# Kernel tuning notes

Hardware: AMD Instinct MI355X
Metric: run time of the kernel (lower is better)

Reference implementation:

```python
import jax, jax.numpy as jnp
import numpy as np

B, N, D = 8, 4096, 6          # clouds, points per cloud, coordinate dim
K = 64                        # max_num_neighbors in radius query
NS1, NS2 = 2048, 512          # fps ratios 0.5 and 0.25
R1, R2 = 0.2, 0.4             # ball-query radii
DIMS = {1: [6, 64, 64, 128], 2: [134, 128, 128, 256], 3: [262, 256, 512, 1024], 4: [1024, 512, 512]}


def setup_inputs():
    key = jax.random.key(0)
    k0, k1, k2 = jax.random.split(key, 3)
    inp = {}
    inp['synapse_cordi'] = jax.random.normal(k0, (B * N, D), jnp.float32)
    inp['batch_index'] = jnp.repeat(jnp.arange(B, dtype=jnp.int32), N)
    inp['weight'] = jax.random.uniform(k1, (B * N,), jnp.float32)
    k = k2
    for i, dims in DIMS.items():
        for j in range(len(dims) - 1):
            k, kw = jax.random.split(k)
            inp[f'w{i}_{j}'] = jax.random.normal(kw, (dims[j], dims[j + 1]), jnp.float32) * (1.0 / float(np.sqrt(dims[j])))
            inp[f'b{i}_{j}'] = jnp.zeros((dims[j + 1],), jnp.float32)
    return inp


def _mlp(x, params):
    # PyG MLP, plain_last=True; batch-norm at default (eval, running stats) is identity
    n = len(params)
    for i, (W, b) in enumerate(params):
        x = x @ W + b
        if i < n - 1:
            x = jax.nn.relu(x)
    return x


def _fps(pos, n_s):
    # farthest point sampling on one cloud [N, D] -> [n_s] indices (deterministic start at 0)
    d0 = jnp.sum((pos - pos[0]) ** 2, axis=-1)
    def step(mind, _):
        nxt = jnp.argmax(mind)
        mind = jnp.minimum(mind, jnp.sum((pos - pos[nxt]) ** 2, axis=-1))
        return mind, nxt
    _, idxs = jax.lax.scan(step, d0, None, length=n_s - 1)
    return jnp.concatenate([jnp.zeros((1,), idxs.dtype), idxs])


def _ball(pos, pos_q, r):
    # radius query: up to K nearest points within r for each query; [n_q,K] idx + validity mask
    d2 = jnp.sum((pos_q[:, None, :] - pos[None, :, :]) ** 2, axis=-1)  # [n_q, N]
    neg = jnp.where(d2 <= r * r, -d2, -jnp.inf)
    vals, nbr = jax.lax.top_k(neg, K)
    return nbr, vals > -jnp.inf


def _sa(x, pos, params, n_s, r):
    # Weight_Sample_Module: fps -> radius -> PointNetConv (gather, MLP, masked max-scatter)
    idx = jax.vmap(lambda p: _fps(p, n_s))(pos)                     # [B, n_s]
    pos_q = jnp.take_along_axis(pos, idx[..., None], axis=1)        # [B, n_s, D]
    nbr, valid = jax.vmap(lambda p, q: _ball(p, q, r))(pos, pos_q)  # [B, n_s, K]
    gather = lambda a: jax.vmap(lambda t, i: t[i])(a, nbr)          # [B, n_s, K, C]
    rel = gather(pos) - pos_q[:, :, None, :]
    feat = rel if x is None else jnp.concatenate([gather(x), rel], axis=-1)
    h = _mlp(feat, params)                                          # [B, n_s, K, C_out]
    h = jnp.where(valid[..., None], h, -jnp.inf)
    return jnp.max(h, axis=2), pos_q                                # max aggregation


def reference(synapse_cordi, batch_index, weight,
              w1_0, b1_0, w1_1, b1_1, w1_2, b1_2,
              w2_0, b2_0, w2_1, b2_1, w2_2, b2_2,
              w3_0, b3_0, w3_1, b3_1, w3_2, b3_2,
              w4_0, b4_0, w4_1, b4_1):
    pos = synapse_cordi.reshape(B, N, D)  # uniform clouds; batch_index = repeat(arange(B), N)
    p1 = [(w1_0, b1_0), (w1_1, b1_1), (w1_2, b1_2)]
    p2 = [(w2_0, b2_0), (w2_1, b2_1), (w2_2, b2_2)]
    p3 = [(w3_0, b3_0), (w3_1, b3_1), (w3_2, b3_2)]
    p4 = [(w4_0, b4_0), (w4_1, b4_1)]
    x1, pos1 = _sa(None, pos, p1, NS1, R1)   # [B, 2048, 128]
    x2, pos2 = _sa(x1, pos1, p2, NS2, R2)    # [B, 512, 256]
    h = _mlp(jnp.concatenate([x2, pos2], axis=-1), p3)  # [B, 512, 1024]
    g = jnp.max(h, axis=1)                   # global max pool -> [B, 1024]
    return _mlp(g, p4)                       # [B, 512]
```

## Files before the change

### kernel.cpp

```cpp
#include <hip/hip_runtime.h>
#include <math.h>

#define B_ 8
#define N_ 4096
#define D_ 6
#define K_ 64
#define NS1_ 2048
#define NS2_ 512

typedef float v2f __attribute__((ext_vector_type(2)));


__device__ __forceinline__ float dist2_rn(const float* __restrict__ a, const float* __restrict__ q) {
    float s = 0.f;
#pragma unroll
    for (int d = 0; d < 6; ++d) {
        float diff = __fsub_rn(a[d], q[d]);
        s = __fadd_rn(s, __fmul_rn(diff, diff));
    }
    return s;
}

__device__ __forceinline__ unsigned mapf(float x) {
    unsigned u = __float_as_uint(x);
    return (u & 0x80000000u) ? ~u : (u | 0x80000000u);
}
__device__ __forceinline__ float unmapf(unsigned u) {
    return __uint_as_float((u & 0x80000000u) ? (u & 0x7FFFFFFFu) : ~u);
}

template <int CTRL>
__device__ __forceinline__ double dppd(double k) {
    int lo = __double2loint(k), hi = __double2hiint(k);
    int nlo = __builtin_amdgcn_update_dpp(lo, lo, CTRL, 0xF, 0xF, false);
    int nhi = __builtin_amdgcn_update_dpp(hi, hi, CTRL, 0xF, 0xF, false);
    return __hiloint2double(nhi, nlo);
}


__device__ __forceinline__ void wait_flag(unsigned* f, int t) {
    if (t == 0) {
        while (__hip_atomic_load(f, __ATOMIC_RELAXED, __HIP_MEMORY_SCOPE_AGENT) == 0u)
            __builtin_amdgcn_s_sleep(32);
        __builtin_amdgcn_fence(__ATOMIC_ACQUIRE, "agent");
    }
    __syncthreads();
}


template <int NP, int NS>
__device__ __forceinline__ void fps_core(float* __restrict__ spos, int* __restrict__ sidx,
                                         double* __restrict__ part, int t) {
#pragma clang fp contract(off)
    constexpr int NT = 256;
    constexpr int P = NP / NT;
    constexpr int HP = P / 2;
    int lane = t & 63, w = t >> 6;

    v2f px2[HP][6];
#pragma unroll
    for (int j = 0; j < HP; ++j)
#pragma unroll
        for (int d = 0; d < 6; ++d) {
            px2[j][d].x = spos[(t + NT * (2 * j)) * 6 + d];
            px2[j][d].y = spos[(t + NT * (2 * j + 1)) * 6 + d];
        }

    float cx[6];
#pragma unroll
    for (int d = 0; d < 6; ++d) cx[d] = spos[d];

    v2f mind2[HP];
    float runv = -1.f;
    int runj = 0;
#pragma unroll
    for (int j = 0; j < HP; ++j) {
        v2f d2 = {0.f, 0.f};
#pragma unroll
        for (int d = 0; d < 6; ++d) {
            v2f df = px2[j][d] - cx[d];
            d2 = d2 + df * df;
        }
        mind2[j] = d2;
        if (d2.x > runv) { runv = d2.x; runj = t + NT * (2 * j); }
        if (d2.y > runv) { runv = d2.y; runj = t + NT * (2 * j + 1); }
    }

    for (int s = 1; s < NS; ++s) {
        double key = __hiloint2double((int)__float_as_uint(runv), (int)(unsigned)(~runj));
        key = fmax(key, dppd<0x111>(key));
        key = fmax(key, dppd<0x112>(key));
        key = fmax(key, dppd<0x114>(key));
        key = fmax(key, dppd<0x118>(key));
        key = fmax(key, dppd<0x142>(key));
        key = fmax(key, dppd<0x143>(key));
        if (lane == 63) part[(s & 1) * 4 + w] = key;
        __syncthreads();
        double kk = part[(s & 1) * 4 + (lane & 3)];
        kk = fmax(kk, dppd<0x111>(kk));
        kk = fmax(kk, dppd<0x112>(kk));
        int nx = ~__builtin_amdgcn_readlane(__double2loint(kk), 3);
        if (t == 0) sidx[s] = nx;

        const float2* sv2 = (const float2*)spos;
        float2 ca = sv2[nx * 3], cb = sv2[nx * 3 + 1], cc = sv2[nx * 3 + 2];
        cx[0] = ca.x; cx[1] = ca.y; cx[2] = cb.x; cx[3] = cb.y; cx[4] = cc.x; cx[5] = cc.y;

        runv = -1.f;
        runj = 0;
#pragma unroll
        for (int j = 0; j < HP; ++j) {
            v2f d2 = {0.f, 0.f};
#pragma unroll
            for (int d = 0; d < 6; ++d) {
                v2f df = px2[j][d] - cx[d];
                d2 = d2 + df * df;
            }
            float mx = fminf(mind2[j].x, d2.x);
            float my = fminf(mind2[j].y, d2.y);
            mind2[j].x = mx;
            mind2[j].y = my;
            if (mx > runv) { runv = mx; runj = t + NT * (2 * j); }
            if (my > runv) { runv = my; runj = t + NT * (2 * j + 1); }
        }
    }
}


template <int NPTS, int S>
__device__ __forceinline__ void ball_scan(const float* __restrict__ sp,
                                          const float* __restrict__ posq,
                                          int* __restrict__ nbr, int* __restrict__ cnt,
                                          float r2, int qid, int tid,
                                          float* __restrict__ sd, unsigned short* __restrict__ si) {
    float q[6];
#pragma unroll
    for (int d = 0; d < 6; ++d) q[d] = posq[(size_t)qid * 6 + d];

    int n = 0;
    float thr = INFINITY;
#pragma unroll 4
    for (int j = 0; j < NPTS; ++j) {
        float d2 = dist2_rn(sp + j * 6, q);
        if (d2 <= r2 && (n < K_ || d2 < thr)) {
            int i = (n < K_) ? n : (K_ - 1);
            if (n < K_) ++n;
            while (i > 0 && sd[(i - 1) * S + tid] > d2) {
                sd[i * S + tid] = sd[(i - 1) * S + tid];
                si[i * S + tid] = si[(i - 1) * S + tid];
                --i;
            }
            sd[i * S + tid] = d2;
            si[i * S + tid] = (unsigned short)j;
            if (n == K_) thr = sd[(K_ - 1) * S + tid];
        }
    }
    cnt[qid] = n;
    for (int i = 0; i < n; ++i) nbr[(size_t)qid * K_ + i] = (int)si[i * S + tid];
}


__global__ __launch_bounds__(256, 1) void stage12_kernel(
        const float* __restrict__ pos, float* __restrict__ pos1,
        int* __restrict__ nbr1, int* __restrict__ cnt1,
        float* __restrict__ pos2, int* __restrict__ nbr2, int* __restrict__ cnt2,
        unsigned* __restrict__ g, unsigned* flags,
        float r2_1, float r2_2) {
    __shared__ union Smem {
        struct { float spos[N_ * 6]; int sidx[NS1_]; double part[8]; } fps;
        struct { float spos[N_ * 6]; float sd[K_ * 128]; unsigned short si[K_ * 128]; } b1;
        struct { float spos[NS1_ * 6]; float sd[K_ * 64]; unsigned short si[K_ * 64]; } b2;
    } sm;
    int t = threadIdx.x;

    if (blockIdx.x < 8) {
        int b = blockIdx.x;
        float* spos = sm.fps.spos;
        int* sidx = sm.fps.sidx;
        double* part = sm.fps.part;

        {
            const float4* src = (const float4*)(pos + (size_t)b * N_ * 6);
            float4* dst = (float4*)spos;
            for (int e = t; e < N_ * 6 / 4; e += 256) dst[e] = src[e];
        }
        if (t == 0) sidx[0] = 0;
        __syncthreads();

        fps_core<N_, NS1_>(spos, sidx, part, t);
        __syncthreads();

        float smp[NS1_ / 256][6];
#pragma unroll
        for (int i = 0; i < NS1_ / 256; ++i) {
            int s = t + 256 * i;
            int ix = sidx[s];
#pragma unroll
            for (int d = 0; d < 6; ++d) smp[i][d] = spos[ix * 6 + d];
        }
#pragma unroll
        for (int i = 0; i < NS1_ / 256; ++i) {
            int s = t + 256 * i;
#pragma unroll
            for (int d = 0; d < 6; ++d) pos1[((size_t)b * NS1_ + s) * 6 + d] = smp[i][d];
        }
        __syncthreads();
        if (t == 0) {
            __threadfence();
            __hip_atomic_store(&flags[b], 1u, __ATOMIC_RELEASE, __HIP_MEMORY_SCOPE_AGENT);
        }

#pragma unroll
        for (int i = 0; i < NS1_ / 256; ++i) {
            int s = t + 256 * i;
#pragma unroll
            for (int d = 0; d < 6; ++d) spos[s * 6 + d] = smp[i][d];
        }
        for (int e = t; e < 1024; e += 256) g[b * 1024 + e] = 0u;
        if (t == 0) sidx[0] = 0;
        __syncthreads();

        fps_core<NS1_, NS2_>(spos, sidx, part, t);
        __syncthreads();

        for (int s = t; s < NS2_; s += 256) {
            int ix = sidx[s];
#pragma unroll
            for (int d = 0; d < 6; ++d) pos2[((size_t)b * NS2_ + s) * 6 + d] = spos[ix * 6 + d];
        }
        __syncthreads();
        if (t == 0) {
            __threadfence();
            __hip_atomic_store(&flags[8 + b], 1u, __ATOMIC_RELEASE, __HIP_MEMORY_SCOPE_AGENT);
        }
    } else if (blockIdx.x < 8 + 128) {
        int blk = blockIdx.x - 8;
        int b = blk >> 4;
        {
            const float4* src = (const float4*)(pos + (size_t)b * N_ * 6);
            float4* dst = (float4*)sm.b1.spos;
            for (int e = t; e < N_ * 6 / 4; e += 256) dst[e] = src[e];
        }
        __syncthreads();
        wait_flag(&flags[b], t);
        if (t < 128) {
            int qid = blk * 128 + t;
            ball_scan<N_, 128>(sm.b1.spos, pos1, nbr1, cnt1, r2_1, qid, t, sm.b1.sd, sm.b1.si);
        }
    } else {
        int blk = blockIdx.x - 136;
        int b = blk >> 3;
        wait_flag(&flags[b], t);
        {
            const float4* src = (const float4*)(pos1 + (size_t)b * NS1_ * 6);
            float4* dst = (float4*)sm.b2.spos;
            for (int e = t; e < NS1_ * 6 / 4; e += 256) dst[e] = src[e];
        }
        __syncthreads();
        wait_flag(&flags[8 + b], t);
        if (t < 64) {
            int qid = blk * 64 + t;
            ball_scan<NS1_, 64>(sm.b2.spos, pos2, nbr2, cnt2, r2_2, qid, t, sm.b2.sd, sm.b2.si);
        }
    }
}


__global__ __launch_bounds__(256) void sa1_kernel(const float* __restrict__ pos,
                                                  const float* __restrict__ pos1,
                                                  const int* __restrict__ nbr1,
                                                  const int* __restrict__ cnt1,
                                                  const float* __restrict__ W1, const float* __restrict__ B1,
                                                  const float* __restrict__ W2, const float* __restrict__ B2,
                                                  const float* __restrict__ W3, const float* __restrict__ B3,
                                                  float* __restrict__ x1) {
    int lane = threadIdx.x & 63;
    int w = threadIdx.x >> 6;
    int qid = blockIdx.x * 4 + w;
    int b = qid / NS1_;
    const float* p = pos + (size_t)b * N_ * 6;
    float q[6];
#pragma unroll
    for (int d = 0; d < 6; ++d) q[d] = pos1[(size_t)qid * 6 + d];
    int c = cnt1[qid];
    float m0 = -INFINITY, m1 = -INFINITY;

    for (int n = 0; n < c; ++n) {
        int j = nbr1[(size_t)qid * K_ + n];
        float rel[6];
#pragma unroll
        for (int d = 0; d < 6; ++d) rel[d] = p[(size_t)j * 6 + d] - q[d];
        float a = B1[lane];
#pragma unroll
        for (int d = 0; d < 6; ++d) a = fmaf(W1[d * 64 + lane], rel[d], a);
        float h1 = fmaxf(a, 0.f);
        float a2 = B2[lane];
        for (int k = 0; k < 64; ++k) {
            float v = __shfl(h1, k, 64);
            a2 = fmaf(W2[k * 64 + lane], v, a2);
        }
        float h2 = fmaxf(a2, 0.f);
        float o0 = B3[lane], o1 = B3[64 + lane];
        for (int k = 0; k < 64; ++k) {
            float v = __shfl(h2, k, 64);
            o0 = fmaf(W3[k * 128 + lane], v, o0);
            o1 = fmaf(W3[k * 128 + 64 + lane], v, o1);
        }
        m0 = fmaxf(m0, o0);
        m1 = fmaxf(m1, o1);
    }
    x1[(size_t)qid * 128 + lane] = m0;
    x1[(size_t)qid * 128 + 64 + lane] = m1;
}


__global__ __launch_bounds__(256) void sa2_conv(const float* __restrict__ pos1, const float* __restrict__ posq,
                                                const int* __restrict__ nbr, const int* __restrict__ cnt,
                                                const float* __restrict__ x1,
                                                const float* __restrict__ W1, const float* __restrict__ B1,
                                                const float* __restrict__ W2, const float* __restrict__ B2,
                                                const float* __restrict__ W3, const float* __restrict__ B3,
                                                float* __restrict__ out) {
    int lane = threadIdx.x & 63;
    int w = threadIdx.x >> 6;
    int qid = blockIdx.x * 4 + w;
    int b = qid / NS2_;
    float q[6];
#pragma unroll
    for (int d = 0; d < 6; ++d) q[d] = posq[(size_t)qid * 6 + d];
    int c = cnt[qid];
    float m0 = -INFINITY, m1 = -INFINITY, m2 = -INFINITY, m3 = -INFINITY;

    for (int n = 0; n < c; ++n) {
        int j = nbr[(size_t)qid * K_ + n];
        size_t row = (size_t)b * NS1_ + j;
        const float* xs = x1 + row * 128;
        float rel[6];
#pragma unroll
        for (int d = 0; d < 6; ++d) rel[d] = pos1[row * 6 + d] - q[d];
        float a0 = B1[lane], a1 = B1[64 + lane];
        for (int k = 0; k < 128; ++k) {
            float v = xs[k];
            a0 = fmaf(W1[k * 128 + lane], v, a0);
            a1 = fmaf(W1[k * 128 + 64 + lane], v, a1);
        }
#pragma unroll
        for (int d = 0; d < 6; ++d) {
            float v = rel[d];
            a0 = fmaf(W1[(128 + d) * 128 + lane], v, a0);
            a1 = fmaf(W1[(128 + d) * 128 + 64 + lane], v, a1);
        }
        float h1a = fmaxf(a0, 0.f), h1b = fmaxf(a1, 0.f);
        float c0 = B2[lane], c1 = B2[64 + lane];
        for (int k = 0; k < 64; ++k) {
            float v = __shfl(h1a, k, 64);
            c0 = fmaf(W2[k * 128 + lane], v, c0);
            c1 = fmaf(W2[k * 128 + 64 + lane], v, c1);
        }
        for (int k = 0; k < 64; ++k) {
            float v = __shfl(h1b, k, 64);
            c0 = fmaf(W2[(64 + k) * 128 + lane], v, c0);
            c1 = fmaf(W2[(64 + k) * 128 + 64 + lane], v, c1);
        }
        float h2a = fmaxf(c0, 0.f), h2b = fmaxf(c1, 0.f);
        float e0 = B3[lane], e1 = B3[64 + lane], e2 = B3[128 + lane], e3 = B3[192 + lane];
        for (int k = 0; k < 64; ++k) {
            float v = __shfl(h2a, k, 64);
            e0 = fmaf(W3[k * 256 + lane], v, e0);
            e1 = fmaf(W3[k * 256 + 64 + lane], v, e1);
            e2 = fmaf(W3[k * 256 + 128 + lane], v, e2);
            e3 = fmaf(W3[k * 256 + 192 + lane], v, e3);
        }
        for (int k = 0; k < 64; ++k) {
            float v = __shfl(h2b, k, 64);
            e0 = fmaf(W3[(64 + k) * 256 + lane], v, e0);
            e1 = fmaf(W3[(64 + k) * 256 + 64 + lane], v, e1);
            e2 = fmaf(W3[(64 + k) * 256 + 128 + lane], v, e2);
            e3 = fmaf(W3[(64 + k) * 256 + 192 + lane], v, e3);
        }
        m0 = fmaxf(m0, e0);
        m1 = fmaxf(m1, e1);
        m2 = fmaxf(m2, e2);
        m3 = fmaxf(m3, e3);
    }
    out[(size_t)qid * 256 + lane] = m0;
    out[(size_t)qid * 256 + 64 + lane] = m1;
    out[(size_t)qid * 256 + 128 + lane] = m2;
    out[(size_t)qid * 256 + 192 + lane] = m3;
}


__global__ __launch_bounds__(256, 1) void mlp3_kernel(const float* __restrict__ x2, const float* __restrict__ pos2,
                                                      const float* __restrict__ W0, const float* __restrict__ B0,
                                                      const float* __restrict__ W1, const float* __restrict__ B1,
                                                      const float* __restrict__ W2, const float* __restrict__ B2,
                                                      unsigned* __restrict__ g) {
    int lane = threadIdx.x & 63;
    int w = threadIdx.x >> 6;
    int qid0 = blockIdx.x * 16 + w * 4;
    int b = qid0 >> 9;

    float xr[4][4];
#pragma unroll
    for (int q = 0; q < 4; ++q)
#pragma unroll
        for (int j = 0; j < 4; ++j) xr[q][j] = x2[(size_t)(qid0 + q) * 256 + j * 64 + lane];

    float a[4][4];
    {
        float4 bv = *(const float4*)&B0[lane * 4];
#pragma unroll
        for (int q = 0; q < 4; ++q) { a[q][0] = bv.x; a[q][1] = bv.y; a[q][2] = bv.z; a[q][3] = bv.w; }
    }
#pragma unroll
    for (int j = 0; j < 4; ++j) {
        for (int k2 = 0; k2 < 64; ++k2) {
            int k = j * 64 + k2;
            float4 wv = *(const float4*)&W0[(size_t)k * 256 + lane * 4];
#pragma unroll
            for (int q = 0; q < 4; ++q) {
                float v = __shfl(xr[q][j], k2, 64);
                a[q][0] = fmaf(wv.x, v, a[q][0]);
                a[q][1] = fmaf(wv.y, v, a[q][1]);
                a[q][2] = fmaf(wv.z, v, a[q][2]);
                a[q][3] = fmaf(wv.w, v, a[q][3]);
            }
        }
    }
#pragma unroll
    for (int d = 0; d < 6; ++d) {
        float4 wv = *(const float4*)&W0[(size_t)(256 + d) * 256 + lane * 4];
#pragma unroll
        for (int q = 0; q < 4; ++q) {
            float v = pos2[(size_t)(qid0 + q) * 6 + d];
            a[q][0] = fmaf(wv.x, v, a[q][0]);
            a[q][1] = fmaf(wv.y, v, a[q][1]);
            a[q][2] = fmaf(wv.z, v, a[q][2]);
            a[q][3] = fmaf(wv.w, v, a[q][3]);
        }
    }
    float h1[4][4];
#pragma unroll
    for (int q = 0; q < 4; ++q)
#pragma unroll
        for (int u = 0; u < 4; ++u) h1[q][u] = fmaxf(a[q][u], 0.f);

    float c[4][8];
    {
        float4 b0 = *(const float4*)&B1[lane * 8];
        float4 b1 = *(const float4*)&B1[lane * 8 + 4];
#pragma unroll
        for (int q = 0; q < 4; ++q) {
            c[q][0] = b0.x; c[q][1] = b0.y; c[q][2] = b0.z; c[q][3] = b0.w;
            c[q][4] = b1.x; c[q][5] = b1.y; c[q][6] = b1.z; c[q][7] = b1.w;
        }
    }
    for (int l = 0; l < 64; ++l) {
#pragma unroll
        for (int r = 0; r < 4; ++r) {
            int k = l * 4 + r;
            float4 w0 = *(const float4*)&W1[(size_t)k * 512 + lane * 8];
            float4 w1 = *(const float4*)&W1[(size_t)k * 512 + lane * 8 + 4];
#pragma unroll
            for (int q = 0; q < 4; ++q) {
                float v = __shfl(h1[q][r], l, 64);
                c[q][0] = fmaf(w0.x, v, c[q][0]);
                c[q][1] = fmaf(w0.y, v, c[q][1]);
                c[q][2] = fmaf(w0.z, v, c[q][2]);
                c[q][3] = fmaf(w0.w, v, c[q][3]);
                c[q][4] = fmaf(w1.x, v, c[q][4]);
                c[q][5] = fmaf(w1.y, v, c[q][5]);
                c[q][6] = fmaf(w1.z, v, c[q][6]);
                c[q][7] = fmaf(w1.w, v, c[q][7]);
            }
        }
    }
    float h2[4][8];
#pragma unroll
    for (int q = 0; q < 4; ++q)
#pragma unroll
        for (int u = 0; u < 8; ++u) h2[q][u] = fmaxf(c[q][u], 0.f);

    float e[4][16];
#pragma unroll
    for (int jj = 0; jj < 4; ++jj) {
        float4 bv = *(const float4*)&B2[lane * 16 + jj * 4];
#pragma unroll
        for (int q = 0; q < 4; ++q) {
            e[q][jj * 4 + 0] = bv.x; e[q][jj * 4 + 1] = bv.y;
            e[q][jj * 4 + 2] = bv.z; e[q][jj * 4 + 3] = bv.w;
        }
    }
    for (int l = 0; l < 64; ++l) {
#pragma unroll
        for (int r = 0; r < 8; ++r) {
            int k = l * 8 + r;
            const float* wp = &W2[(size_t)k * 1024 + lane * 16];
            float4 w0 = *(const float4*)&wp[0];
            float4 w1 = *(const float4*)&wp[4];
            float4 w2 = *(const float4*)&wp[8];
            float4 w3 = *(const float4*)&wp[12];
#pragma unroll
            for (int q = 0; q < 4; ++q) {
                float v = __shfl(h2[q][r], l, 64);
                e[q][0]  = fmaf(w0.x, v, e[q][0]);
                e[q][1]  = fmaf(w0.y, v, e[q][1]);
                e[q][2]  = fmaf(w0.z, v, e[q][2]);
                e[q][3]  = fmaf(w0.w, v, e[q][3]);
                e[q][4]  = fmaf(w1.x, v, e[q][4]);
                e[q][5]  = fmaf(w1.y, v, e[q][5]);
                e[q][6]  = fmaf(w1.z, v, e[q][6]);
                e[q][7]  = fmaf(w1.w, v, e[q][7]);
                e[q][8]  = fmaf(w2.x, v, e[q][8]);
                e[q][9]  = fmaf(w2.y, v, e[q][9]);
                e[q][10] = fmaf(w2.z, v, e[q][10]);
                e[q][11] = fmaf(w2.w, v, e[q][11]);
                e[q][12] = fmaf(w3.x, v, e[q][12]);
                e[q][13] = fmaf(w3.y, v, e[q][13]);
                e[q][14] = fmaf(w3.z, v, e[q][14]);
                e[q][15] = fmaf(w3.w, v, e[q][15]);
            }
        }
    }
#pragma unroll
    for (int u = 0; u < 16; ++u) {
        float m = fmaxf(fmaxf(e[0][u], e[1][u]), fmaxf(e[2][u], e[3][u]));
        atomicMax(&g[b * 1024 + lane * 16 + u], mapf(m));
    }
}


__global__ __launch_bounds__(512) void mlp4_kernel(const unsigned* __restrict__ g,
                                                   const float* __restrict__ W0, const float* __restrict__ B0,
                                                   const float* __restrict__ W1, const float* __restrict__ B1,
                                                   float* __restrict__ out) {
    int b = blockIdx.x;
    int c = threadIdx.x;
    __shared__ float h[512];
    float a = B0[c];
    for (int k = 0; k < 1024; ++k) {
        float v = unmapf(g[b * 1024 + k]);
        a = fmaf(v, W0[k * 512 + c], a);
    }
    h[c] = fmaxf(a, 0.f);
    __syncthreads();
    float o = B1[c];
    for (int k = 0; k < 512; ++k) o = fmaf(h[k], W1[k * 512 + c], o);
    out[(size_t)b * 512 + c] = o;
}


extern "C" void kernel_launch(void* const* d_in, const int* in_sizes, int n_in,
                              void* d_out, int out_size, void* d_ws, size_t ws_size,
                              hipStream_t stream) {
    const float* pos = (const float*)d_in[0];
    const float* w1_0 = (const float*)d_in[3];
    const float* b1_0 = (const float*)d_in[4];
    const float* w1_1 = (const float*)d_in[5];
    const float* b1_1 = (const float*)d_in[6];
    const float* w1_2 = (const float*)d_in[7];
    const float* b1_2 = (const float*)d_in[8];
    const float* w2_0 = (const float*)d_in[9];
    const float* b2_0 = (const float*)d_in[10];
    const float* w2_1 = (const float*)d_in[11];
    const float* b2_1 = (const float*)d_in[12];
    const float* w2_2 = (const float*)d_in[13];
    const float* b2_2 = (const float*)d_in[14];
    const float* w3_0 = (const float*)d_in[15];
    const float* b3_0 = (const float*)d_in[16];
    const float* w3_1 = (const float*)d_in[17];
    const float* b3_1 = (const float*)d_in[18];
    const float* w3_2 = (const float*)d_in[19];
    const float* b3_2 = (const float*)d_in[20];
    const float* w4_0 = (const float*)d_in[21];
    const float* b4_0 = (const float*)d_in[22];
    const float* w4_1 = (const float*)d_in[23];
    const float* b4_1 = (const float*)d_in[24];
    float* out = (float*)d_out;

    char* ws = (char*)d_ws;
    size_t off = 0;
    float* pos1 = (float*)(ws + off);  off += (size_t)B_ * NS1_ * 6 * 4;
    int* nbr1 = (int*)(ws + off);      off += (size_t)B_ * NS1_ * K_ * 4;
    int* cnt1 = (int*)(ws + off);      off += (size_t)B_ * NS1_ * 4;
    float* x1 = (float*)(ws + off);    off += (size_t)B_ * NS1_ * 128 * 4;
    float* pos2 = (float*)(ws + off);  off += (size_t)B_ * NS2_ * 6 * 4;
    int* nbr2 = (int*)(ws + off);      off += (size_t)B_ * NS2_ * K_ * 4;
    int* cnt2 = (int*)(ws + off);      off += (size_t)B_ * NS2_ * 4;
    float* x2 = (float*)(ws + off);    off += (size_t)B_ * NS2_ * 256 * 4;
    unsigned* g = (unsigned*)(ws + off); off += (size_t)B_ * 1024 * 4;
    unsigned* flags = (unsigned*)(ws + off); off += 64;

    const float r2_1 = (float)(0.2 * 0.2);
    const float r2_2 = (float)(0.4 * 0.4);

    hipMemsetAsync(flags, 0, 64, stream);

    stage12_kernel<<<200, 256, 0, stream>>>(pos, pos1, nbr1, cnt1, pos2, nbr2, cnt2, g,
                                            flags, r2_1, r2_2);
    sa1_kernel<<<(B_ * NS1_) / 4, 256, 0, stream>>>(pos, pos1, nbr1, cnt1,
                                                    w1_0, b1_0, w1_1, b1_1, w1_2, b1_2, x1);
    sa2_conv<<<(B_ * NS2_) / 4, 256, 0, stream>>>(pos1, pos2, nbr2, cnt2, x1,
                                                  w2_0, b2_0, w2_1, b2_1, w2_2, b2_2, x2);
    mlp3_kernel<<<(B_ * NS2_) / 16, 256, 0, stream>>>(x2, pos2, w3_0, b3_0, w3_1, b3_1, w3_2, b3_2, g);
    mlp4_kernel<<<B_, 512, 0, stream>>>(g, w4_0, b4_0, w4_1, b4_1, out);
}
```

Before: 2.497 ms.

## Fuse SA1 MLP into ball-query blocks and SA2 conv into MLP3 kernel

```diff
diff --git a/kernel.cpp b/kernel.cpp
--- a/kernel.cpp
+++ b/kernel.cpp
@@ -128,11 +128,10 @@
 
 
 template <int NPTS, int S>
-__device__ __forceinline__ void ball_scan(const float* __restrict__ sp,
-                                          const float* __restrict__ posq,
-                                          int* __restrict__ nbr, int* __restrict__ cnt,
-                                          float r2, int qid, int tid,
-                                          float* __restrict__ sd, unsigned short* __restrict__ si) {
+__device__ __forceinline__ int ball_scan(const float* __restrict__ sp,
+                                         const float* __restrict__ posq,
+                                         float r2, int qid, int tid,
+                                         float* __restrict__ sd, unsigned short* __restrict__ si) {
     float q[6];
 #pragma unroll
     for (int d = 0; d < 6; ++d) q[d] = posq[(size_t)qid * 6 + d];
@@ -155,23 +154,26 @@
             if (n == K_) thr = sd[(K_ - 1) * S + tid];
         }
     }
-    cnt[qid] = n;
-    for (int i = 0; i < n; ++i) nbr[(size_t)qid * K_ + i] = (int)si[i * S + tid];
+    return n;
 }
 
 
 __global__ __launch_bounds__(256, 1) void stage12_kernel(
-        const float* __restrict__ pos, float* __restrict__ pos1,
-        int* __restrict__ nbr1, int* __restrict__ cnt1,
-        float* __restrict__ pos2, int* __restrict__ nbr2, int* __restrict__ cnt2,
+        const float* __restrict__ pos, float* __restrict__ pos1, float* __restrict__ pos2,
+        float* __restrict__ x1, int* __restrict__ nbr2, int* __restrict__ cnt2,
         unsigned* __restrict__ g, unsigned* flags,
+        const float* __restrict__ W1_0, const float* __restrict__ B1_0,
+        const float* __restrict__ W1_1, const float* __restrict__ B1_1,
+        const float* __restrict__ W1_2, const float* __restrict__ B1_2,
         float r2_1, float r2_2) {
     __shared__ union Smem {
         struct { float spos[N_ * 6]; int sidx[NS1_]; double part[8]; } fps;
-        struct { float spos[N_ * 6]; float sd[K_ * 128]; unsigned short si[K_ * 128]; } b1;
-        struct { float spos[NS1_ * 6]; float sd[K_ * 64]; unsigned short si[K_ * 64]; } b2;
+        struct { float spos[N_ * 6]; float sd[K_ * 128]; unsigned short si[K_ * 128];
+                 unsigned short scnt[128]; } p1;
+        struct { float spos1[NS1_ * 6]; float sd2[K_ * 64]; unsigned short si2[K_ * 64]; } b2;
     } sm;
     int t = threadIdx.x;
+    int lane = t & 63, w = t >> 6;
 
     if (blockIdx.x < 8) {
         int b = blockIdx.x;
@@ -238,14 +240,53 @@
         int b = blk >> 4;
         {
             const float4* src = (const float4*)(pos + (size_t)b * N_ * 6);
-            float4* dst = (float4*)sm.b1.spos;
+            float4* dst = (float4*)sm.p1.spos;
             for (int e = t; e < N_ * 6 / 4; e += 256) dst[e] = src[e];
         }
         __syncthreads();
         wait_flag(&flags[b], t);
+
+        int qbase1 = b * NS1_ + (blk & 15) * 128;
         if (t < 128) {
-            int qid = blk * 128 + t;
-            ball_scan<N_, 128>(sm.b1.spos, pos1, nbr1, cnt1, r2_1, qid, t, sm.b1.sd, sm.b1.si);
+            int n = ball_scan<N_, 128>(sm.p1.spos, pos1, r2_1, qbase1 + t, t, sm.p1.sd, sm.p1.si);
+            sm.p1.scnt[t] = (unsigned short)n;
+        }
+        __syncthreads();
+
+        for (int qq = 0; qq < 32; ++qq) {
+            int lq = w * 32 + qq;
+            int qid = qbase1 + lq;
+            float q[6];
+#pragma unroll
+            for (int d = 0; d < 6; ++d) q[d] = pos1[(size_t)qid * 6 + d];
+            int c = sm.p1.scnt[lq];
+            float m0 = -INFINITY, m1 = -INFINITY;
+            for (int n = 0; n < c; ++n) {
+                int j = sm.p1.si[n * 128 + lq];
+                float rel[6];
+#pragma unroll
+                for (int d = 0; d < 6; ++d) rel[d] = sm.p1.spos[j * 6 + d] - q[d];
+                float a = B1_0[lane];
+#pragma unroll
+                for (int d = 0; d < 6; ++d) a = fmaf(W1_0[d * 64 + lane], rel[d], a);
+                float h1 = fmaxf(a, 0.f);
+                float a2 = B1_1[lane];
+                for (int k = 0; k < 64; ++k) {
+                    float v = __shfl(h1, k, 64);
+                    a2 = fmaf(W1_1[k * 64 + lane], v, a2);
+                }
+                float h2 = fmaxf(a2, 0.f);
+                float o0 = B1_2[lane], o1 = B1_2[64 + lane];
+                for (int k = 0; k < 64; ++k) {
+                    float v = __shfl(h2, k, 64);
+                    o0 = fmaf(W1_2[k * 128 + lane], v, o0);
+                    o1 = fmaf(W1_2[k * 128 + 64 + lane], v, o1);
+                }
+                m0 = fmaxf(m0, o0);
+                m1 = fmaxf(m1, o1);
+            }
+            x1[(size_t)qid * 128 + lane] = m0;
+            x1[(size_t)qid * 128 + 64 + lane] = m1;
         }
     } else {
         int blk = blockIdx.x - 136;
@@ -253,162 +294,117 @@
         wait_flag(&flags[b], t);
         {
             const float4* src = (const float4*)(pos1 + (size_t)b * NS1_ * 6);
-            float4* dst = (float4*)sm.b2.spos;
+            float4* dst = (float4*)sm.b2.spos1;
             for (int e = t; e < NS1_ * 6 / 4; e += 256) dst[e] = src[e];
         }
         __syncthreads();
         wait_flag(&flags[8 + b], t);
         if (t < 64) {
             int qid = blk * 64 + t;
-            ball_scan<NS1_, 64>(sm.b2.spos, pos2, nbr2, cnt2, r2_2, qid, t, sm.b2.sd, sm.b2.si);
-        }
-    }
-}
-
-
-__global__ __launch_bounds__(256) void sa1_kernel(const float* __restrict__ pos,
-                                                  const float* __restrict__ pos1,
-                                                  const int* __restrict__ nbr1,
-                                                  const int* __restrict__ cnt1,
-                                                  const float* __restrict__ W1, const float* __restrict__ B1,
-                                                  const float* __restrict__ W2, const float* __restrict__ B2,
-                                                  const float* __restrict__ W3, const float* __restrict__ B3,
-                                                  float* __restrict__ x1) {
+            int n = ball_scan<NS1_, 64>(sm.b2.spos1, pos2, r2_2, qid, t, sm.b2.sd2, sm.b2.si2);
+            cnt2[qid] = n;
+            for (int i = 0; i < n; ++i) nbr2[(size_t)qid * K_ + i] = (int)sm.b2.si2[i * 64 + t];
+        }
+    }
+}
+
+
+__global__ __launch_bounds__(256, 1) void sa2_mlp3_kernel(
+        const float* __restrict__ pos1, const float* __restrict__ pos2,
+        const int* __restrict__ nbr, const int* __restrict__ cnt,
+        const float* __restrict__ x1,
+        const float* __restrict__ W1, const float* __restrict__ B1,
+        const float* __restrict__ W2, const float* __restrict__ B2,
+        const float* __restrict__ W3, const float* __restrict__ B3,
+        const float* __restrict__ M0, const float* __restrict__ MB0,
+        const float* __restrict__ M1, const float* __restrict__ MB1,
+        const float* __restrict__ M2, const float* __restrict__ MB2,
+        unsigned* __restrict__ g) {
+    __shared__ float sx2[16 * 256];
     int lane = threadIdx.x & 63;
     int w = threadIdx.x >> 6;
-    int qid = blockIdx.x * 4 + w;
-    int b = qid / NS1_;
-    const float* p = pos + (size_t)b * N_ * 6;
-    float q[6];
-#pragma unroll
-    for (int d = 0; d < 6; ++d) q[d] = pos1[(size_t)qid * 6 + d];
-    int c = cnt1[qid];
-    float m0 = -INFINITY, m1 = -INFINITY;
-
-    for (int n = 0; n < c; ++n) {
-        int j = nbr1[(size_t)qid * K_ + n];
-        float rel[6];
-#pragma unroll
-        for (int d = 0; d < 6; ++d) rel[d] = p[(size_t)j * 6 + d] - q[d];
-        float a = B1[lane];
-#pragma unroll
-        for (int d = 0; d < 6; ++d) a = fmaf(W1[d * 64 + lane], rel[d], a);
-        float h1 = fmaxf(a, 0.f);
-        float a2 = B2[lane];
-        for (int k = 0; k < 64; ++k) {
-            float v = __shfl(h1, k, 64);
-            a2 = fmaf(W2[k * 64 + lane], v, a2);
-        }
-        float h2 = fmaxf(a2, 0.f);
-        float o0 = B3[lane], o1 = B3[64 + lane];
-        for (int k = 0; k < 64; ++k) {
-            float v = __shfl(h2, k, 64);
-            o0 = fmaf(W3[k * 128 + lane], v, o0);
-            o1 = fmaf(W3[k * 128 + 64 + lane], v, o1);
-        }
-        m0 = fmaxf(m0, o0);
-        m1 = fmaxf(m1, o1);
-    }
-    x1[(size_t)qid * 128 + lane] = m0;
-    x1[(size_t)qid * 128 + 64 + lane] = m1;
-}
-
-
-__global__ __launch_bounds__(256) void sa2_conv(const float* __restrict__ pos1, const float* __restrict__ posq,
-                                                const int* __restrict__ nbr, const int* __restrict__ cnt,
-                                                const float* __restrict__ x1,
-                                                const float* __restrict__ W1, const float* __restrict__ B1,
-                                                const float* __restrict__ W2, const float* __restrict__ B2,
-                                                const float* __restrict__ W3, const float* __restrict__ B3,
-                                                float* __restrict__ out) {
-    int lane = threadIdx.x & 63;
-    int w = threadIdx.x >> 6;
-    int qid = blockIdx.x * 4 + w;
-    int b = qid / NS2_;
-    float q[6];
-#pragma unroll
-    for (int d = 0; d < 6; ++d) q[d] = posq[(size_t)qid * 6 + d];
-    int c = cnt[qid];
-    float m0 = -INFINITY, m1 = -INFINITY, m2 = -INFINITY, m3 = -INFINITY;
-
-    for (int n = 0; n < c; ++n) {
-        int j = nbr[(size_t)qid * K_ + n];
-        size_t row = (size_t)b * NS1_ + j;
-        const float* xs = x1 + row * 128;
-        float rel[6];
-#pragma unroll
-        for (int d = 0; d < 6; ++d) rel[d] = pos1[row * 6 + d] - q[d];
-        float a0 = B1[lane], a1 = B1[64 + lane];
-        for (int k = 0; k < 128; ++k) {
-            float v = xs[k];
-            a0 = fmaf(W1[k * 128 + lane], v, a0);
-            a1 = fmaf(W1[k * 128 + 64 + lane], v, a1);
-        }
-#pragma unroll
-        for (int d = 0; d < 6; ++d) {
-            float v = rel[d];
-            a0 = fmaf(W1[(128 + d) * 128 + lane], v, a0);
-            a1 = fmaf(W1[(128 + d) * 128 + 64 + lane], v, a1);
-        }
-        float h1a = fmaxf(a0, 0.f), h1b = fmaxf(a1, 0.f);
-        float c0 = B2[lane], c1 = B2[64 + lane];
-        for (int k = 0; k < 64; ++k) {
-            float v = __shfl(h1a, k, 64);
-            c0 = fmaf(W2[k * 128 + lane], v, c0);
-            c1 = fmaf(W2[k * 128 + 64 + lane], v, c1);
-        }
-        for (int k = 0; k < 64; ++k) {
-            float v = __shfl(h1b, k, 64);
-            c0 = fmaf(W2[(64 + k) * 128 + lane], v, c0);
-            c1 = fmaf(W2[(64 + k) * 128 + 64 + lane], v, c1);
-        }
-        float h2a = fmaxf(c0, 0.f), h2b = fmaxf(c1, 0.f);
-        float e0 = B3[lane], e1 = B3[64 + lane], e2 = B3[128 + lane], e3 = B3[192 + lane];
-        for (int k = 0; k < 64; ++k) {
-            float v = __shfl(h2a, k, 64);
-            e0 = fmaf(W3[k * 256 + lane], v, e0);
-            e1 = fmaf(W3[k * 256 + 64 + lane], v, e1);
-            e2 = fmaf(W3[k * 256 + 128 + lane], v, e2);
-            e3 = fmaf(W3[k * 256 + 192 + lane], v, e3);
-        }
-        for (int k = 0; k < 64; ++k) {
-            float v = __shfl(h2b, k, 64);
-            e0 = fmaf(W3[(64 + k) * 256 + lane], v, e0);
-            e1 = fmaf(W3[(64 + k) * 256 + 64 + lane], v, e1);
-            e2 = fmaf(W3[(64 + k) * 256 + 128 + lane], v, e2);
-            e3 = fmaf(W3[(64 + k) * 256 + 192 + lane], v, e3);
-        }
-        m0 = fmaxf(m0, e0);
-        m1 = fmaxf(m1, e1);
-        m2 = fmaxf(m2, e2);
-        m3 = fmaxf(m3, e3);
-    }
-    out[(size_t)qid * 256 + lane] = m0;
-    out[(size_t)qid * 256 + 64 + lane] = m1;
-    out[(size_t)qid * 256 + 128 + lane] = m2;
-    out[(size_t)qid * 256 + 192 + lane] = m3;
-}
-
-
-__global__ __launch_bounds__(256, 1) void mlp3_kernel(const float* __restrict__ x2, const float* __restrict__ pos2,
-                                                      const float* __restrict__ W0, const float* __restrict__ B0,
-                                                      const float* __restrict__ W1, const float* __restrict__ B1,
-                                                      const float* __restrict__ W2, const float* __restrict__ B2,
-                                                      unsigned* __restrict__ g) {
-    int lane = threadIdx.x & 63;
-    int w = threadIdx.x >> 6;
-    int qid0 = blockIdx.x * 16 + w * 4;
-    int b = qid0 >> 9;
+    int qbase = blockIdx.x * 16;
+    int b = qbase >> 9;
+
+    for (int qq = 0; qq < 4; ++qq) {
+        int lq = w * 4 + qq;
+        int qid = qbase + lq;
+        float q[6];
+#pragma unroll
+        for (int d = 0; d < 6; ++d) q[d] = pos2[(size_t)qid * 6 + d];
+        int c = cnt[qid];
+        float m0 = -INFINITY, m1 = -INFINITY, m2 = -INFINITY, m3 = -INFINITY;
+        for (int n = 0; n < c; ++n) {
+            int j = nbr[(size_t)qid * K_ + n];
+            size_t row = (size_t)b * NS1_ + j;
+            const float* xs = x1 + row * 128;
+            float rel[6];
+#pragma unroll
+            for (int d = 0; d < 6; ++d) rel[d] = pos1[row * 6 + d] - q[d];
+            float a0 = B1[lane], a1 = B1[64 + lane];
+            for (int k = 0; k < 128; ++k) {
+                float v = xs[k];
+                a0 = fmaf(W1[k * 128 + lane], v, a0);
+                a1 = fmaf(W1[k * 128 + 64 + lane], v, a1);
+            }
+#pragma unroll
+            for (int d = 0; d < 6; ++d) {
+                float v = rel[d];
+                a0 = fmaf(W1[(128 + d) * 128 + lane], v, a0);
+                a1 = fmaf(W1[(128 + d) * 128 + 64 + lane], v, a1);
+            }
+            float h1a = fmaxf(a0, 0.f), h1b = fmaxf(a1, 0.f);
+            float c0 = B2[lane], c1 = B2[64 + lane];
+            for (int k = 0; k < 64; ++k) {
+                float v = __shfl(h1a, k, 64);
+                c0 = fmaf(W2[k * 128 + lane], v, c0);
+                c1 = fmaf(W2[k * 128 + 64 + lane], v, c1);
+            }
+            for (int k = 0; k < 64; ++k) {
+                float v = __shfl(h1b, k, 64);
+                c0 = fmaf(W2[(64 + k) * 128 + lane], v, c0);
+                c1 = fmaf(W2[(64 + k) * 128 + 64 + lane], v, c1);
+            }
+            float h2a = fmaxf(c0, 0.f), h2b = fmaxf(c1, 0.f);
+            float e0 = B3[lane], e1 = B3[64 + lane], e2 = B3[128 + lane], e3 = B3[192 + lane];
+            for (int k = 0; k < 64; ++k) {
+                float v = __shfl(h2a, k, 64);
+                e0 = fmaf(W3[k * 256 + lane], v, e0);
+                e1 = fmaf(W3[k * 256 + 64 + lane], v, e1);
+                e2 = fmaf(W3[k * 256 + 128 + lane], v, e2);
+                e3 = fmaf(W3[k * 256 + 192 + lane], v, e3);
+            }
+            for (int k = 0; k < 64; ++k) {
+                float v = __shfl(h2b, k, 64);
+                e0 = fmaf(W3[(64 + k) * 256 + lane], v, e0);
+                e1 = fmaf(W3[(64 + k) * 256 + 64 + lane], v, e1);
+                e2 = fmaf(W3[(64 + k) * 256 + 128 + lane], v, e2);
+                e3 = fmaf(W3[(64 + k) * 256 + 192 + lane], v, e3);
+            }
+            m0 = fmaxf(m0, e0);
+            m1 = fmaxf(m1, e1);
+            m2 = fmaxf(m2, e2);
+            m3 = fmaxf(m3, e3);
+        }
+        sx2[lq * 256 + lane] = m0;
+        sx2[lq * 256 + 64 + lane] = m1;
+        sx2[lq * 256 + 128 + lane] = m2;
+        sx2[lq * 256 + 192 + lane] = m3;
+    }
+    __syncthreads();
+
+    int lq0 = w * 4;
+    int qid0 = qbase + lq0;
 
     float xr[4][4];
 #pragma unroll
     for (int q = 0; q < 4; ++q)
 #pragma unroll
-        for (int j = 0; j < 4; ++j) xr[q][j] = x2[(size_t)(qid0 + q) * 256 + j * 64 + lane];
+        for (int j = 0; j < 4; ++j) xr[q][j] = sx2[(lq0 + q) * 256 + j * 64 + lane];
 
     float a[4][4];
     {
-        float4 bv = *(const float4*)&B0[lane * 4];
+        float4 bv = *(const float4*)&MB0[lane * 4];
 #pragma unroll
         for (int q = 0; q < 4; ++q) { a[q][0] = bv.x; a[q][1] = bv.y; a[q][2] = bv.z; a[q][3] = bv.w; }
     }
@@ -416,7 +412,7 @@
     for (int j = 0; j < 4; ++j) {
         for (int k2 = 0; k2 < 64; ++k2) {
             int k = j * 64 + k2;
-            float4 wv = *(const float4*)&W0[(size_t)k * 256 + lane * 4];
+            float4 wv = *(const float4*)&M0[(size_t)k * 256 + lane * 4];
 #pragma unroll
             for (int q = 0; q < 4; ++q) {
                 float v = __shfl(xr[q][j], k2, 64);
@@ -429,7 +425,7 @@
     }
 #pragma unroll
     for (int d = 0; d < 6; ++d) {
-        float4 wv = *(const float4*)&W0[(size_t)(256 + d) * 256 + lane * 4];
+        float4 wv = *(const float4*)&M0[(size_t)(256 + d) * 256 + lane * 4];
 #pragma unroll
         for (int q = 0; q < 4; ++q) {
             float v = pos2[(size_t)(qid0 + q) * 6 + d];
@@ -447,8 +443,8 @@
 
     float c[4][8];
     {
-        float4 b0 = *(const float4*)&B1[lane * 8];
-        float4 b1 = *(const float4*)&B1[lane * 8 + 4];
+        float4 b0 = *(const float4*)&MB1[lane * 8];
+        float4 b1 = *(const float4*)&MB1[lane * 8 + 4];
 #pragma unroll
         for (int q = 0; q < 4; ++q) {
             c[q][0] = b0.x; c[q][1] = b0.y; c[q][2] = b0.z; c[q][3] = b0.w;
@@ -459,8 +455,8 @@
 #pragma unroll
         for (int r = 0; r < 4; ++r) {
             int k = l * 4 + r;
-            float4 w0 = *(const float4*)&W1[(size_t)k * 512 + lane * 8];
-            float4 w1 = *(const float4*)&W1[(size_t)k * 512 + lane * 8 + 4];
+            float4 w0 = *(const float4*)&M1[(size_t)k * 512 + lane * 8];
+            float4 w1 = *(const float4*)&M1[(size_t)k * 512 + lane * 8 + 4];
 #pragma unroll
             for (int q = 0; q < 4; ++q) {
                 float v = __shfl(h1[q][r], l, 64);
@@ -484,7 +480,7 @@
     float e[4][16];
 #pragma unroll
     for (int jj = 0; jj < 4; ++jj) {
-        float4 bv = *(const float4*)&B2[lane * 16 + jj * 4];
+        float4 bv = *(const float4*)&MB2[lane * 16 + jj * 4];
 #pragma unroll
         for (int q = 0; q < 4; ++q) {
             e[q][jj * 4 + 0] = bv.x; e[q][jj * 4 + 1] = bv.y;
@@ -495,7 +491,7 @@
 #pragma unroll
         for (int r = 0; r < 8; ++r) {
             int k = l * 8 + r;
-            const float* wp = &W2[(size_t)k * 1024 + lane * 16];
+            const float* wp = &M2[(size_t)k * 1024 + lane * 16];
             float4 w0 = *(const float4*)&wp[0];
             float4 w1 = *(const float4*)&wp[4];
             float4 w2 = *(const float4*)&wp[8];
@@ -580,28 +576,24 @@
 
     char* ws = (char*)d_ws;
     size_t off = 0;
-    float* pos1 = (float*)(ws + off);  off += (size_t)B_ * NS1_ * 6 * 4;
-    int* nbr1 = (int*)(ws + off);      off += (size_t)B_ * NS1_ * K_ * 4;
-    int* cnt1 = (int*)(ws + off);      off += (size_t)B_ * NS1_ * 4;
-    float* x1 = (float*)(ws + off);    off += (size_t)B_ * NS1_ * 128 * 4;
-    float* pos2 = (float*)(ws + off);  off += (size_t)B_ * NS2_ * 6 * 4;
-    int* nbr2 = (int*)(ws + off);      off += (size_t)B_ * NS2_ * K_ * 4;
-    int* cnt2 = (int*)(ws + off);      off += (size_t)B_ * NS2_ * 4;
-    float* x2 = (float*)(ws + off);    off += (size_t)B_ * NS2_ * 256 * 4;
+    float* pos1 = (float*)(ws + off);    off += (size_t)B_ * NS1_ * 6 * 4;
+    float* pos2 = (float*)(ws + off);    off += (size_t)B_ * NS2_ * 6 * 4;
+    float* x1 = (float*)(ws + off);      off += (size_t)B_ * NS1_ * 128 * 4;
+    int* nbr2 = (int*)(ws + off);        off += (size_t)B_ * NS2_ * K_ * 4;
+    int* cnt2 = (int*)(ws + off);        off += (size_t)B_ * NS2_ * 4;
     unsigned* g = (unsigned*)(ws + off); off += (size_t)B_ * 1024 * 4;
-    unsigned* flags = (unsigned*)(ws + off); off += 64;
+    unsigned* flags = (unsigned*)(ws + off); off += 16 * 4;
 
     const float r2_1 = (float)(0.2 * 0.2);
     const float r2_2 = (float)(0.4 * 0.4);
 
-    hipMemsetAsync(flags, 0, 64, stream);
-
-    stage12_kernel<<<200, 256, 0, stream>>>(pos, pos1, nbr1, cnt1, pos2, nbr2, cnt2, g,
-                                            flags, r2_1, r2_2);
-    sa1_kernel<<<(B_ * NS1_) / 4, 256, 0, stream>>>(pos, pos1, nbr1, cnt1,
-                                                    w1_0, b1_0, w1_1, b1_1, w1_2, b1_2, x1);
-    sa2_conv<<<(B_ * NS2_) / 4, 256, 0, stream>>>(pos1, pos2, nbr2, cnt2, x1,
-                                                  w2_0, b2_0, w2_1, b2_1, w2_2, b2_2, x2);
-    mlp3_kernel<<<(B_ * NS2_) / 16, 256, 0, stream>>>(x2, pos2, w3_0, b3_0, w3_1, b3_1, w3_2, b3_2, g);
+    hipMemsetAsync(flags, 0, 16 * 4, stream);
+
+    stage12_kernel<<<200, 256, 0, stream>>>(pos, pos1, pos2, x1, nbr2, cnt2, g, flags,
+                                            w1_0, b1_0, w1_1, b1_1, w1_2, b1_2,
+                                            r2_1, r2_2);
+    sa2_mlp3_kernel<<<(B_ * NS2_) / 16, 256, 0, stream>>>(pos1, pos2, nbr2, cnt2, x1,
+                                                          w2_0, b2_0, w2_1, b2_1, w2_2, b2_2,
+                                                          w3_0, b3_0, w3_1, b3_1, w3_2, b3_2, g);
     mlp4_kernel<<<B_, 512, 0, stream>>>(g, w4_0, b4_0, w4_1, b4_1, out);
 }
```

Result: no change. 2.509 ms (+0.5%).
